# Kernel tuning notes

Hardware: AMD Instinct MI355X
Metric: run time of the kernel (lower is better)

## Reference

```python
import jax, jax.numpy as jnp
import numpy as np

N_HEADS = 16
HEAD_SIZE = 64
SEQ_LEN = 2048
EMBED = 1024
BATCH = 2


def setup_inputs() -> dict:
    key = jax.random.key(0)
    ks = jax.random.split(key, 9)
    d_inner = N_HEADS * HEAD_SIZE
    s = 1.0 / np.sqrt(EMBED)
    inp = {
        "inputs": jax.random.normal(ks[0], (BATCH, SEQ_LEN, EMBED), jnp.float32),
        "Wq": jax.random.uniform(ks[1], (EMBED, d_inner), jnp.float32, -s, s),
        "bq": jax.random.uniform(ks[2], (d_inner,), jnp.float32, -s, s),
        "Wk": jax.random.uniform(ks[3], (EMBED, d_inner), jnp.float32, -s, s),
        "bk": jax.random.uniform(ks[4], (d_inner,), jnp.float32, -s, s),
        "Wv": jax.random.uniform(ks[5], (EMBED, d_inner), jnp.float32, -s, s),
        "bv": jax.random.uniform(ks[6], (d_inner,), jnp.float32, -s, s),
        "Wo": jax.random.uniform(ks[7], (d_inner, EMBED), jnp.float32, -s, s),
        "bo": jax.random.uniform(ks[8], (EMBED,), jnp.float32, -s, s),
    }
    return inp


def reference(inputs, Wq, bq, Wk, bk, Wv, bv, Wo, bo):
    B, S, _ = inputs.shape
    # QKV projections -> [B, H, S, Dh]
    def proj(W, b):
        return (inputs @ W + b).reshape(B, S, N_HEADS, HEAD_SIZE).transpose(0, 2, 1, 3)
    q, k, v = proj(Wq, bq), proj(Wk, bk), proj(Wv, bv)
    scores = jnp.einsum("bhqd,bhkd->bhqk", q, k) / jnp.sqrt(jnp.float32(HEAD_SIZE))
    causal = jnp.tril(jnp.ones((S, S), dtype=bool))  # [S, S]
    scores = jnp.where(causal[None, None], scores, -jnp.inf)
    attn = jax.nn.softmax(scores, axis=-1)  # dropout is identity in eval
    out = jnp.einsum("bhqk,bhkd->bhqd", attn, v)
    out = out.transpose(0, 2, 1, 3).reshape(B, S, N_HEADS * HEAD_SIZE)
    return out @ Wo + bo
```

## Files before the change

kernel.cpp:

```cpp
#include <hip/hip_runtime.h>
#include <hip/hip_bf16.h>
#include <math.h>

#define NH 16
#define DH 64
#define SEQ 2048
#define EMBED 1024
#define DINNER 1024
#define BATCH 2
#define MTOK 4096

typedef __bf16 bf16x8 __attribute__((ext_vector_type(8)));
typedef float  f32x4  __attribute__((ext_vector_type(4)));
typedef float  f32x16 __attribute__((ext_vector_type(16)));
typedef unsigned int u32;

__device__ __forceinline__ void gload16(const void* g, void* l) {
    __builtin_amdgcn_global_load_lds((const __attribute__((address_space(1))) void*)g,
                                     (__attribute__((address_space(3))) void*)l, 16, 0, 0);
}

__global__ __launch_bounds__(256) void cvt_bf16(
    const float* __restrict__ src, __bf16* __restrict__ dst, int n)
{
    int i = (blockIdx.x * 256 + threadIdx.x) * 4;
    if (i + 3 < n) {
        float4 v = *(const float4*)&src[i];
        dst[i + 0] = (__bf16)v.x;
        dst[i + 1] = (__bf16)v.y;
        dst[i + 2] = (__bf16)v.z;
        dst[i + 3] = (__bf16)v.w;
    }
}

__global__ __launch_bounds__(256) void tconv4(
    const float* __restrict__ W0, const float* __restrict__ W1,
    const float* __restrict__ W2, const float* __restrict__ W3,
    __bf16* __restrict__ D0, __bf16* __restrict__ D1,
    __bf16* __restrict__ D2, __bf16* __restrict__ D3)
{
    const int z = blockIdx.z;
    const float* __restrict__ src = (z == 0) ? W0 : (z == 1) ? W1 : (z == 2) ? W2 : W3;
    __bf16* __restrict__ dst      = (z == 0) ? D0 : (z == 1) ? D1 : (z == 2) ? D2 : D3;
    const int R = 1024, C = 1024;

    __shared__ float t[32][33];
    const int c0 = blockIdx.x * 32, r0 = blockIdx.y * 32;
    const int x = threadIdx.x & 31, y = threadIdx.x >> 5;
#pragma unroll
    for (int i = 0; i < 4; ++i)
        t[y + 8 * i][x] = src[(size_t)(r0 + y + 8 * i) * C + c0 + x];
    __syncthreads();
#pragma unroll
    for (int i = 0; i < 4; ++i)
        dst[(size_t)(c0 + y + 8 * i) * R + r0 + x] = (__bf16)t[x][y + 8 * i];
}

#define QSCALE 0.18033688f

__global__ __launch_bounds__(256) void gemm128(
    const __bf16* __restrict__ A,
    const __bf16* __restrict__ Bt0, const __bf16* __restrict__ Bt1, const __bf16* __restrict__ Bt2,
    const float* __restrict__ b0, const float* __restrict__ b1, const float* __restrict__ b2,
    void* __restrict__ o0, void* __restrict__ o1, void* __restrict__ o2,
    int Kdim, int mode3)
{
    const int z = blockIdx.z;
    const __bf16* __restrict__ Bt = (z == 0) ? Bt0 : (z == 1) ? Bt1 : Bt2;
    const float*  __restrict__ bias = (z == 0) ? b0 : (z == 1) ? b1 : b2;
    void* __restrict__ outp = (z == 0) ? o0 : (z == 1) ? o1 : o2;
    const int mode = mode3 ? 3 : z;
    const float scale = (mode == 0) ? QSCALE : 1.0f;

    __shared__ __bf16 As[128 * 32];
    __shared__ __bf16 Bs[128 * 32];

    const int tid  = threadIdx.x;
    const int lane = tid & 63;
    const int wid  = tid >> 6;
    const int wm = wid >> 1, wn = wid & 1;
    const int ls = lane & 15, lg = lane >> 4;
    const int m0 = blockIdx.y * 128, n0 = blockIdx.x * 128;

    const int sr = tid >> 2;
    const int sc = (tid & 3) * 8;

    f32x4 acc[4][4] = {};

    for (int k0 = 0; k0 < Kdim; k0 += 32) {
        gload16(&A [(size_t)(m0 + sr)      * Kdim + k0 + sc], &As[sr * 32 + sc]);
        gload16(&A [(size_t)(m0 + 64 + sr) * Kdim + k0 + sc], &As[(64 + sr) * 32 + sc]);
        gload16(&Bt[(size_t)(n0 + sr)      * Kdim + k0 + sc], &Bs[sr * 32 + sc]);
        gload16(&Bt[(size_t)(n0 + 64 + sr) * Kdim + k0 + sc], &Bs[(64 + sr) * 32 + sc]);
        __syncthreads();

        bf16x8 af[4], bfr[4];
#pragma unroll
        for (int i = 0; i < 4; ++i) {
            af[i]  = *(const bf16x8*)&As[(wm * 64 + i * 16 + ls) * 32 + lg * 8];
            bfr[i] = *(const bf16x8*)&Bs[(wn * 64 + i * 16 + ls) * 32 + lg * 8];
        }
#pragma unroll
        for (int i = 0; i < 4; ++i)
#pragma unroll
            for (int jx = 0; jx < 4; ++jx)
                acc[i][jx] = __builtin_amdgcn_mfma_f32_16x16x32_bf16(af[i], bfr[jx], acc[i][jx], 0, 0, 0);
        __syncthreads();
    }

#pragma unroll
    for (int i = 0; i < 4; ++i) {
#pragma unroll
        for (int jx = 0; jx < 4; ++jx) {
#pragma unroll
            for (int j = 0; j < 4; ++j) {
                const int m = m0 + wm * 64 + i * 16 + lg * 4 + j;
                const int n = n0 + wn * 64 + jx * 16 + ls;
                const float v = (acc[i][jx][j] + bias[n]) * scale;
                if (mode == 3) {
                    ((float*)outp)[(size_t)m * EMBED + n] = v;
                } else {
                    const int b = m >> 11, s = m & 2047;
                    const int h = n >> 6,  d = n & 63;
                    if (mode == 2)
                        ((__bf16*)outp)[(((size_t)(b * NH + h) * DH + d) << 11) + s] = (__bf16)v;
                    else
                        ((__bf16*)outp)[((((size_t)(b * NH + h) << 11) + s) * DH) + d] = (__bf16)v;
                }
            }
        }
    }
}

__global__ __launch_bounds__(256) void attn_mfma(
    const __bf16* __restrict__ Q, const __bf16* __restrict__ K,
    const __bf16* __restrict__ Vt, __bf16* __restrict__ ctx)
{
    __shared__ __bf16 lds[2][8192];

    const int tid  = threadIdx.x;
    const int wave = tid >> 6;
    const int lane = tid & 63;
    const int col  = lane & 31;
    const int hi   = lane >> 5;
    const int bh  = blockIdx.x & 31;
    const int qtb = 15 - (blockIdx.x >> 5);
    const int qb  = qtb * 128;
    const int qlo = qb + wave * 32;
    const int b = bh >> 4, h = bh & 15;

    const __bf16* __restrict__ Qb = Q + ((size_t)bh << 11) * DH;
    const char* __restrict__ Kg = (const char*)(K  + ((size_t)bh << 11) * DH);
    const char* __restrict__ Vg = (const char*)(Vt + ((size_t)bh << 11) * DH);

    const int srow = tid >> 3;
    const int scb  = (tid & 7) * 16;
    const int sswz = scb ^ ((srow & 7) << 4);

    bf16x8 qf[4];
#pragma unroll
    for (int c = 0; c < 4; ++c)
        qf[c] = *(const bf16x8*)&Qb[(size_t)(qlo + col) * DH + c * 16 + hi * 8];

    const int nt = 2 * qtb + 2;

#pragma unroll
    for (int i = 0; i < 2; ++i) {
        const int row = i * 32 + srow;
        gload16(Kg + (size_t)row * 128 + sswz,
                (char*)&lds[0][0] + i * 4096 + tid * 16);
        gload16(Vg + (size_t)row * 4096 + sswz,
                (char*)&lds[0][4096] + i * 4096 + tid * 16);
    }
    __syncthreads();

    f32x16 oT0 = {}, oT1 = {};
    float mrun = -INFINITY, lrun = 0.f;
    int cur = 0;
    const int swz = (col & 7) << 4;

    for (int t = 0; t < nt; ++t) {
        if (t + 1 < nt) {
            const int kbn = (t + 1) * 64;
#pragma unroll
            for (int i = 0; i < 2; ++i) {
                const int row = i * 32 + srow;
                gload16(Kg + (size_t)(kbn + row) * 128 + sswz,
                        (char*)&lds[cur ^ 1][0] + i * 4096 + tid * 16);
                gload16(Vg + (size_t)row * 4096 + (size_t)kbn * 2 + sswz,
                        (char*)&lds[cur ^ 1][4096] + i * 4096 + tid * 16);
            }
        }

        const int kb = t * 64;
        const char* ldsK = (const char*)&lds[cur][0];
        const char* ldsV = (const char*)&lds[cur][4096];

#pragma unroll
        for (int sub = 0; sub < 2; ++sub) {
            const int k0 = kb + sub * 32;
            if (k0 > qlo + 31) break;

            bf16x8 kf[4];
            const int krow = sub * 32 + col;
#pragma unroll
            for (int c = 0; c < 4; ++c)
                kf[c] = *(const bf16x8*)(ldsK + krow * 128 + ((c * 32 + hi * 16) ^ swz));

            f32x16 st = {};
#pragma unroll
            for (int c = 0; c < 4; ++c)
                st = __builtin_amdgcn_mfma_f32_32x32x16_bf16(kf[c], qf[c], st, 0, 0, 0);

            if (k0 + 31 > qlo) {
#pragma unroll
                for (int r = 0; r < 16; ++r) {
                    const int krel = (r & 3) + 8 * (r >> 2) + 4 * hi;
                    if (k0 + krel > qlo + col) st[r] = -INFINITY;
                }
            }

            float t0 = fmaxf(fmaxf(fmaxf(st[0], st[1]), fmaxf(st[2], st[3])),
                             fmaxf(fmaxf(st[4], st[5]), fmaxf(st[6], st[7])));
            float t1 = fmaxf(fmaxf(fmaxf(st[8], st[9]),  fmaxf(st[10], st[11])),
                             fmaxf(fmaxf(st[12], st[13]), fmaxf(st[14], st[15])));
            float tmax = fmaxf(t0, t1);
            tmax = fmaxf(tmax, __shfl_xor(tmax, 32));

            if (__any(tmax > mrun + 8.f)) {
                const float mnew = fmaxf(mrun, tmax);
                const float corr = exp2f(mrun - mnew);
                lrun *= corr;
                oT0 *= corr;
                oT1 *= corr;
                mrun = mnew;
            }

            float p[16];
#pragma unroll
            for (int r = 0; r < 16; ++r) p[r] = exp2f(st[r] - mrun);
            float ps0 = ((p[0] + p[1]) + (p[2] + p[3])) + ((p[4] + p[5]) + (p[6] + p[7]));
            float ps1 = ((p[8] + p[9]) + (p[10] + p[11])) + ((p[12] + p[13]) + (p[14] + p[15]));
            float psum = ps0 + ps1;
            psum += __shfl_xor(psum, 32);
            lrun += psum;

            u32 w_[8];
#pragma unroll
            for (int i = 0; i < 8; ++i) {
                u32 r_;
                asm("v_cvt_pk_bf16_f32 %0, %1, %2" : "=v"(r_) : "v"(p[2 * i]), "v"(p[2 * i + 1]));
                w_[i] = r_;
            }
            asm("v_permlane32_swap_b32 %0, %1" : "+v"(w_[0]), "+v"(w_[2]));
            asm("v_permlane32_swap_b32 %0, %1" : "+v"(w_[1]), "+v"(w_[3]));
            asm("v_permlane32_swap_b32 %0, %1" : "+v"(w_[4]), "+v"(w_[6]));
            asm("v_permlane32_swap_b32 %0, %1" : "+v"(w_[5]), "+v"(w_[7]));

            union { u32 u[4]; bf16x8 v; } c0_, c1_;
            c0_.u[0] = w_[0]; c0_.u[1] = w_[1]; c0_.u[2] = w_[2]; c0_.u[3] = w_[3];
            c1_.u[0] = w_[4]; c1_.u[1] = w_[5]; c1_.u[2] = w_[6]; c1_.u[3] = w_[7];

            const int s0b = (sub * 2) * 32;
            bf16x8 v00 = *(const bf16x8*)(ldsV + (     col) * 128 + ((s0b      + hi * 16) ^ swz));
            bf16x8 v01 = *(const bf16x8*)(ldsV + (     col) * 128 + ((s0b + 32 + hi * 16) ^ swz));
            bf16x8 v10 = *(const bf16x8*)(ldsV + (32 + col) * 128 + ((s0b      + hi * 16) ^ swz));
            bf16x8 v11 = *(const bf16x8*)(ldsV + (32 + col) * 128 + ((s0b + 32 + hi * 16) ^ swz));
            oT0 = __builtin_amdgcn_mfma_f32_32x32x16_bf16(v00, c0_.v, oT0, 0, 0, 0);
            oT0 = __builtin_amdgcn_mfma_f32_32x32x16_bf16(v01, c1_.v, oT0, 0, 0, 0);
            oT1 = __builtin_amdgcn_mfma_f32_32x32x16_bf16(v10, c0_.v, oT1, 0, 0, 0);
            oT1 = __builtin_amdgcn_mfma_f32_32x32x16_bf16(v11, c1_.v, oT1, 0, 0, 0);
        }

        __syncthreads();
        cur ^= 1;
    }

    const float inv = 1.0f / lrun;
    const size_t base = ((size_t)(b * SEQ + qlo + col)) * DINNER + h * 64;
#pragma unroll
    for (int g = 0; g < 4; ++g) {
        __bf16 t4[4];
#pragma unroll
        for (int j = 0; j < 4; ++j) t4[j] = (__bf16)(oT0[4 * g + j] * inv);
        *(uint2*)&ctx[base + 8 * g + 4 * hi] = *(uint2*)t4;
#pragma unroll
        for (int j = 0; j < 4; ++j) t4[j] = (__bf16)(oT1[4 * g + j] * inv);
        *(uint2*)&ctx[base + 32 + 8 * g + 4 * hi] = *(uint2*)t4;
    }
}

extern "C" void kernel_launch(void* const* d_in, const int* in_sizes, int n_in,
                              void* d_out, int out_size, void* d_ws, size_t ws_size,
                              hipStream_t stream)
{
    const float* X  = (const float*)d_in[0];
    const float* Wq = (const float*)d_in[1];
    const float* bq = (const float*)d_in[2];
    const float* Wk = (const float*)d_in[3];
    const float* bk = (const float*)d_in[4];
    const float* Wv = (const float*)d_in[5];
    const float* bv = (const float*)d_in[6];
    const float* Wo = (const float*)d_in[7];
    const float* bo = (const float*)d_in[8];
    float* out = (float*)d_out;

    __bf16* ws  = (__bf16*)d_ws;
    const size_t MI = 1048576;
    __bf16* Xb   = ws;
    __bf16* Wtq  = ws + 4  * MI;
    __bf16* Wtk  = ws + 5  * MI;
    __bf16* Wtv  = ws + 6  * MI;
    __bf16* Wto  = ws + 7  * MI;
    __bf16* Qb   = ws + 8  * MI;
    __bf16* Kb   = ws + 12 * MI;
    __bf16* Vtb  = ws + 16 * MI;
    __bf16* ctxb = ws + 20 * MI;

    cvt_bf16<<<dim3(MTOK * EMBED / 1024), dim3(256), 0, stream>>>(X, Xb, MTOK * EMBED);
    tconv4<<<dim3(32, 32, 4), dim3(256), 0, stream>>>(Wq, Wk, Wv, Wo, Wtq, Wtk, Wtv, Wto);

    {
        dim3 grid(DINNER / 128, MTOK / 128, 3), blk(256);
        gemm128<<<grid, blk, 0, stream>>>(Xb, Wtq, Wtk, Wtv, bq, bk, bv,
                                          Qb, Kb, Vtb, EMBED, 0);
    }

    {
        dim3 grid(32 * (SEQ / 128)), blk(256);
        attn_mfma<<<grid, blk, 0, stream>>>(Qb, Kb, Vtb, ctxb);
    }

    {
        dim3 grid(EMBED / 128, MTOK / 128, 1), blk(256);
        gemm128<<<grid, blk, 0, stream>>>(ctxb, Wto, Wto, Wto, bo, bo, bo,
                                          out, out, out, DINNER, 1);
    }
}
```

Baseline: 152.6 us.

## Shrink attention blocks to 64 queries and process full 64-key tiles per step

The attention kernel now uses 128-thread blocks covering 64 query rows instead of 256 threads covering 128, doubling the grid to 1024 blocks to improve load balance across the causal triangle. Each iteration computes scores for the full 64-key tile in one pass (two 32-wide MFMA chains) with one softmax update, instead of two sequential 32-key sub-steps. The K/V staging loops were adjusted to four 16-row loads per thread. In exchange, each K/V tile is loaded by more blocks, raising global traffic, and register pressure per wave increases. Diagonal tiles now compute fully masked halves instead of skipping them.

Result: no change. 150.3 us (-1.5%).

```diff
diff --git a/kernel.cpp b/kernel.cpp
--- a/kernel.cpp
+++ b/kernel.cpp
@@ -132,7 +132,7 @@
     }
 }
 
-__global__ __launch_bounds__(256) void attn_mfma(
+__global__ __launch_bounds__(128) void attn_mfma(
     const __bf16* __restrict__ Q, const __bf16* __restrict__ K,
     const __bf16* __restrict__ Vt, __bf16* __restrict__ ctx)
 {
@@ -143,9 +143,9 @@
     const int lane = tid & 63;
     const int col  = lane & 31;
     const int hi   = lane >> 5;
-    const int bh  = blockIdx.x & 31;
-    const int qtb = 15 - (blockIdx.x >> 5);
-    const int qb  = qtb * 128;
+    const int bh = blockIdx.x & 31;
+    const int qt = 31 - (blockIdx.x >> 5);
+    const int qb  = qt * 64;
     const int qlo = qb + wave * 32;
     const int b = bh >> 4, h = bh & 15;
 
@@ -154,23 +154,22 @@
     const char* __restrict__ Vg = (const char*)(Vt + ((size_t)bh << 11) * DH);
 
     const int srow = tid >> 3;
-    const int scb  = (tid & 7) * 16;
-    const int sswz = scb ^ ((srow & 7) << 4);
+    const int sswz = ((tid & 7) * 16) ^ ((srow & 7) << 4);
 
     bf16x8 qf[4];
 #pragma unroll
     for (int c = 0; c < 4; ++c)
         qf[c] = *(const bf16x8*)&Qb[(size_t)(qlo + col) * DH + c * 16 + hi * 8];
 
-    const int nt = 2 * qtb + 2;
-
-#pragma unroll
-    for (int i = 0; i < 2; ++i) {
-        const int row = i * 32 + srow;
+    const int nt = qt + 1;
+
+#pragma unroll
+    for (int i = 0; i < 4; ++i) {
+        const int row = i * 16 + srow;
         gload16(Kg + (size_t)row * 128 + sswz,
-                (char*)&lds[0][0] + i * 4096 + tid * 16);
+                (char*)&lds[0][0] + i * 2048 + tid * 16);
         gload16(Vg + (size_t)row * 4096 + sswz,
-                (char*)&lds[0][4096] + i * 4096 + tid * 16);
+                (char*)&lds[0][0] + 8192 + i * 2048 + tid * 16);
     }
     __syncthreads();
 
@@ -183,93 +182,107 @@
         if (t + 1 < nt) {
             const int kbn = (t + 1) * 64;
 #pragma unroll
-            for (int i = 0; i < 2; ++i) {
-                const int row = i * 32 + srow;
+            for (int i = 0; i < 4; ++i) {
+                const int row = i * 16 + srow;
                 gload16(Kg + (size_t)(kbn + row) * 128 + sswz,
-                        (char*)&lds[cur ^ 1][0] + i * 4096 + tid * 16);
+                        (char*)&lds[cur ^ 1][0] + i * 2048 + tid * 16);
                 gload16(Vg + (size_t)row * 4096 + (size_t)kbn * 2 + sswz,
-                        (char*)&lds[cur ^ 1][4096] + i * 4096 + tid * 16);
+                        (char*)&lds[cur ^ 1][0] + 8192 + i * 2048 + tid * 16);
             }
         }
 
-        const int kb = t * 64;
+        const int k0 = t * 64;
         const char* ldsK = (const char*)&lds[cur][0];
-        const char* ldsV = (const char*)&lds[cur][4096];
-
-#pragma unroll
-        for (int sub = 0; sub < 2; ++sub) {
-            const int k0 = kb + sub * 32;
-            if (k0 > qlo + 31) break;
-
-            bf16x8 kf[4];
-            const int krow = sub * 32 + col;
-#pragma unroll
-            for (int c = 0; c < 4; ++c)
-                kf[c] = *(const bf16x8*)(ldsK + krow * 128 + ((c * 32 + hi * 16) ^ swz));
-
-            f32x16 st = {};
-#pragma unroll
-            for (int c = 0; c < 4; ++c)
-                st = __builtin_amdgcn_mfma_f32_32x32x16_bf16(kf[c], qf[c], st, 0, 0, 0);
-
-            if (k0 + 31 > qlo) {
-#pragma unroll
-                for (int r = 0; r < 16; ++r) {
-                    const int krel = (r & 3) + 8 * (r >> 2) + 4 * hi;
-                    if (k0 + krel > qlo + col) st[r] = -INFINITY;
-                }
+        const char* ldsV = ldsK + 8192;
+
+        bf16x8 kfa[4], kfb[4];
+#pragma unroll
+        for (int c = 0; c < 4; ++c) {
+            kfa[c] = *(const bf16x8*)(ldsK + (     col) * 128 + ((c * 32 + hi * 16) ^ swz));
+            kfb[c] = *(const bf16x8*)(ldsK + (32 + col) * 128 + ((c * 32 + hi * 16) ^ swz));
+        }
+
+        f32x16 sta = {}, stb = {};
+#pragma unroll
+        for (int c = 0; c < 4; ++c) {
+            sta = __builtin_amdgcn_mfma_f32_32x32x16_bf16(kfa[c], qf[c], sta, 0, 0, 0);
+            stb = __builtin_amdgcn_mfma_f32_32x32x16_bf16(kfb[c], qf[c], stb, 0, 0, 0);
+        }
+
+        if (k0 + 63 > qlo) {
+#pragma unroll
+            for (int r = 0; r < 16; ++r) {
+                const int krel = (r & 3) + 8 * (r >> 2) + 4 * hi;
+                if (k0 + krel > qlo + col)      sta[r] = -INFINITY;
+                if (k0 + 32 + krel > qlo + col) stb[r] = -INFINITY;
             }
-
-            float t0 = fmaxf(fmaxf(fmaxf(st[0], st[1]), fmaxf(st[2], st[3])),
-                             fmaxf(fmaxf(st[4], st[5]), fmaxf(st[6], st[7])));
-            float t1 = fmaxf(fmaxf(fmaxf(st[8], st[9]),  fmaxf(st[10], st[11])),
-                             fmaxf(fmaxf(st[12], st[13]), fmaxf(st[14], st[15])));
-            float tmax = fmaxf(t0, t1);
-            tmax = fmaxf(tmax, __shfl_xor(tmax, 32));
-
-            if (__any(tmax > mrun + 8.f)) {
-                const float mnew = fmaxf(mrun, tmax);
-                const float corr = exp2f(mrun - mnew);
-                lrun *= corr;
-                oT0 *= corr;
-                oT1 *= corr;
-                mrun = mnew;
-            }
-
-            float p[16];
-#pragma unroll
-            for (int r = 0; r < 16; ++r) p[r] = exp2f(st[r] - mrun);
-            float ps0 = ((p[0] + p[1]) + (p[2] + p[3])) + ((p[4] + p[5]) + (p[6] + p[7]));
-            float ps1 = ((p[8] + p[9]) + (p[10] + p[11])) + ((p[12] + p[13]) + (p[14] + p[15]));
-            float psum = ps0 + ps1;
-            psum += __shfl_xor(psum, 32);
-            lrun += psum;
-
-            u32 w_[8];
-#pragma unroll
-            for (int i = 0; i < 8; ++i) {
-                u32 r_;
-                asm("v_cvt_pk_bf16_f32 %0, %1, %2" : "=v"(r_) : "v"(p[2 * i]), "v"(p[2 * i + 1]));
-                w_[i] = r_;
-            }
-            asm("v_permlane32_swap_b32 %0, %1" : "+v"(w_[0]), "+v"(w_[2]));
-            asm("v_permlane32_swap_b32 %0, %1" : "+v"(w_[1]), "+v"(w_[3]));
-            asm("v_permlane32_swap_b32 %0, %1" : "+v"(w_[4]), "+v"(w_[6]));
-            asm("v_permlane32_swap_b32 %0, %1" : "+v"(w_[5]), "+v"(w_[7]));
-
-            union { u32 u[4]; bf16x8 v; } c0_, c1_;
-            c0_.u[0] = w_[0]; c0_.u[1] = w_[1]; c0_.u[2] = w_[2]; c0_.u[3] = w_[3];
-            c1_.u[0] = w_[4]; c1_.u[1] = w_[5]; c1_.u[2] = w_[6]; c1_.u[3] = w_[7];
-
-            const int s0b = (sub * 2) * 32;
-            bf16x8 v00 = *(const bf16x8*)(ldsV + (     col) * 128 + ((s0b      + hi * 16) ^ swz));
-            bf16x8 v01 = *(const bf16x8*)(ldsV + (     col) * 128 + ((s0b + 32 + hi * 16) ^ swz));
-            bf16x8 v10 = *(const bf16x8*)(ldsV + (32 + col) * 128 + ((s0b      + hi * 16) ^ swz));
-            bf16x8 v11 = *(const bf16x8*)(ldsV + (32 + col) * 128 + ((s0b + 32 + hi * 16) ^ swz));
-            oT0 = __builtin_amdgcn_mfma_f32_32x32x16_bf16(v00, c0_.v, oT0, 0, 0, 0);
-            oT0 = __builtin_amdgcn_mfma_f32_32x32x16_bf16(v01, c1_.v, oT0, 0, 0, 0);
-            oT1 = __builtin_amdgcn_mfma_f32_32x32x16_bf16(v10, c0_.v, oT1, 0, 0, 0);
-            oT1 = __builtin_amdgcn_mfma_f32_32x32x16_bf16(v11, c1_.v, oT1, 0, 0, 0);
+        }
+
+        float ta = fmaxf(fmaxf(fmaxf(sta[0], sta[1]), fmaxf(sta[2], sta[3])),
+                         fmaxf(fmaxf(sta[4], sta[5]), fmaxf(sta[6], sta[7])));
+        float tb = fmaxf(fmaxf(fmaxf(sta[8], sta[9]),  fmaxf(sta[10], sta[11])),
+                         fmaxf(fmaxf(sta[12], sta[13]), fmaxf(sta[14], sta[15])));
+        float tc = fmaxf(fmaxf(fmaxf(stb[0], stb[1]), fmaxf(stb[2], stb[3])),
+                         fmaxf(fmaxf(stb[4], stb[5]), fmaxf(stb[6], stb[7])));
+        float td = fmaxf(fmaxf(fmaxf(stb[8], stb[9]),  fmaxf(stb[10], stb[11])),
+                         fmaxf(fmaxf(stb[12], stb[13]), fmaxf(stb[14], stb[15])));
+        float tmax = fmaxf(fmaxf(ta, tb), fmaxf(tc, td));
+        tmax = fmaxf(tmax, __shfl_xor(tmax, 32));
+
+        if (__any(tmax > mrun + 8.f)) {
+            const float mnew = fmaxf(mrun, tmax);
+            const float corr = exp2f(mrun - mnew);
+            lrun *= corr;
+            oT0 *= corr;
+            oT1 *= corr;
+            mrun = mnew;
+        }
+
+        float pa[16], pb[16];
+#pragma unroll
+        for (int r = 0; r < 16; ++r) { pa[r] = exp2f(sta[r] - mrun); pb[r] = exp2f(stb[r] - mrun); }
+        float psa = (((pa[0] + pa[1]) + (pa[2] + pa[3])) + ((pa[4] + pa[5]) + (pa[6] + pa[7])))
+                  + (((pa[8] + pa[9]) + (pa[10] + pa[11])) + ((pa[12] + pa[13]) + (pa[14] + pa[15])));
+        float psb = (((pb[0] + pb[1]) + (pb[2] + pb[3])) + ((pb[4] + pb[5]) + (pb[6] + pb[7])))
+                  + (((pb[8] + pb[9]) + (pb[10] + pb[11])) + ((pb[12] + pb[13]) + (pb[14] + pb[15])));
+        float psum = psa + psb;
+        psum += __shfl_xor(psum, 32);
+        lrun += psum;
+
+        u32 wa[8], wb[8];
+#pragma unroll
+        for (int i = 0; i < 8; ++i) {
+            u32 r1, r2;
+            asm("v_cvt_pk_bf16_f32 %0, %1, %2" : "=v"(r1) : "v"(pa[2 * i]), "v"(pa[2 * i + 1]));
+            asm("v_cvt_pk_bf16_f32 %0, %1, %2" : "=v"(r2) : "v"(pb[2 * i]), "v"(pb[2 * i + 1]));
+            wa[i] = r1; wb[i] = r2;
+        }
+        asm("v_permlane32_swap_b32 %0, %1" : "+v"(wa[0]), "+v"(wa[2]));
+        asm("v_permlane32_swap_b32 %0, %1" : "+v"(wa[1]), "+v"(wa[3]));
+        asm("v_permlane32_swap_b32 %0, %1" : "+v"(wa[4]), "+v"(wa[6]));
+        asm("v_permlane32_swap_b32 %0, %1" : "+v"(wa[5]), "+v"(wa[7]));
+        asm("v_permlane32_swap_b32 %0, %1" : "+v"(wb[0]), "+v"(wb[2]));
+        asm("v_permlane32_swap_b32 %0, %1" : "+v"(wb[1]), "+v"(wb[3]));
+        asm("v_permlane32_swap_b32 %0, %1" : "+v"(wb[4]), "+v"(wb[6]));
+        asm("v_permlane32_swap_b32 %0, %1" : "+v"(wb[5]), "+v"(wb[7]));
+
+        union { u32 u[4]; bf16x8 v; } cA0, cA1, cB0, cB1;
+        cA0.u[0] = wa[0]; cA0.u[1] = wa[1]; cA0.u[2] = wa[2]; cA0.u[3] = wa[3];
+        cA1.u[0] = wa[4]; cA1.u[1] = wa[5]; cA1.u[2] = wa[6]; cA1.u[3] = wa[7];
+        cB0.u[0] = wb[0]; cB0.u[1] = wb[1]; cB0.u[2] = wb[2]; cB0.u[3] = wb[3];
+        cB1.u[0] = wb[4]; cB1.u[1] = wb[5]; cB1.u[2] = wb[6]; cB1.u[3] = wb[7];
+
+#pragma unroll
+        for (int dh = 0; dh < 2; ++dh) {
+            bf16x8 v0 = *(const bf16x8*)(ldsV + (dh * 32 + col) * 128 + ((0  + hi * 16) ^ swz));
+            bf16x8 v1 = *(const bf16x8*)(ldsV + (dh * 32 + col) * 128 + ((32 + hi * 16) ^ swz));
+            bf16x8 v2 = *(const bf16x8*)(ldsV + (dh * 32 + col) * 128 + ((64 + hi * 16) ^ swz));
+            bf16x8 v3 = *(const bf16x8*)(ldsV + (dh * 32 + col) * 128 + ((96 + hi * 16) ^ swz));
+            f32x16& o = dh ? oT1 : oT0;
+            o = __builtin_amdgcn_mfma_f32_32x32x16_bf16(v0, cA0.v, o, 0, 0, 0);
+            o = __builtin_amdgcn_mfma_f32_32x32x16_bf16(v1, cA1.v, o, 0, 0, 0);
+            o = __builtin_amdgcn_mfma_f32_32x32x16_bf16(v2, cB0.v, o, 0, 0, 0);
+            o = __builtin_amdgcn_mfma_f32_32x32x16_bf16(v3, cB1.v, o, 0, 0, 0);
         }
 
         __syncthreads();
@@ -327,7 +340,7 @@
     }
 
     {
-        dim3 grid(32 * (SEQ / 128)), blk(256);
+        dim3 grid(32 * (SEQ / 64)), blk(128);
         attn_mfma<<<grid, blk, 0, stream>>>(Qb, Kb, Vtb, ctxb);
     }
 
```
